# Kernel optimization log

Hardware: AMD Instinct MI355X
Metric: run time of the kernel (lower is better)

The kernel has to match this reference:

```python
import jax, jax.numpy as jnp
import numpy as np

B, S, D, H, SEP = 4, 2048, 768, 8, 102
Dh = D // H


def layer_norm(x, g, b, eps=1e-5):
    m = jnp.mean(x, axis=-1, keepdims=True)
    v = jnp.var(x, axis=-1, keepdims=True)
    return (x - m) / jnp.sqrt(v + eps) * g + b


def setup_inputs() -> dict:
    key = jax.random.key(0)
    ks = jax.random.split(key, 16)
    hidden_states = jax.random.normal(ks[0], (B, S, D), dtype=jnp.float32)
    # input_ids: random vocab ids avoiding SEP, with two SEP tokens planted per row
    rng = np.random.default_rng(0)
    ids = rng.integers(103, 30000, size=(B, S))
    for b in range(B):
        ids[b, S // 3 + 7 * b] = SEP
        ids[b, 2 * S // 3 + 11 * b] = SEP
    input_ids = jnp.asarray(ids, dtype=jnp.int64)
    attention_mask = jnp.ones((B, S), dtype=jnp.int32)
    sc = 0.02
    p = {}
    p['Wq'] = jax.random.normal(ks[1], (D, D), jnp.float32) * sc
    p['bq'] = jnp.zeros((D,), jnp.float32)
    p['Wk'] = jax.random.normal(ks[2], (D, D), jnp.float32) * sc
    p['bk'] = jnp.zeros((D,), jnp.float32)
    p['Wv'] = jax.random.normal(ks[3], (D, D), jnp.float32) * sc
    p['bv'] = jnp.zeros((D,), jnp.float32)
    p['Wo'] = jax.random.normal(ks[4], (D, D), jnp.float32) * sc
    p['bo'] = jnp.zeros((D,), jnp.float32)
    p['ln1_g'] = jnp.ones((D,), jnp.float32)
    p['ln1_b'] = jnp.zeros((D,), jnp.float32)
    p['W1'] = jax.random.normal(ks[5], (D, D), jnp.float32) * sc  # d_ff = d_model
    p['b1'] = jnp.zeros((D,), jnp.float32)
    p['W2'] = jax.random.normal(ks[6], (D, D), jnp.float32) * sc
    p['b2'] = jnp.zeros((D,), jnp.float32)
    p['ln2_g'] = jnp.ones((D,), jnp.float32)
    p['ln2_b'] = jnp.zeros((D,), jnp.float32)
    p['dn_g'] = jnp.ones((D,), jnp.float32)
    p['dn_b'] = jnp.zeros((D,), jnp.float32)
    return dict(hidden_states=hidden_states, input_ids=input_ids,
                attention_mask=attention_mask, **p)


def reference(hidden_states, input_ids, attention_mask,
              Wq, bq, Wk, bk, Wv, bv, Wo, bo, ln1_g, ln1_b,
              W1, b1, W2, b2, ln2_g, ln2_b, dn_g, dn_b):
    x = hidden_states
    # --- SEP-based ragged segment discovery (vectorized over batch) ---
    sep = input_ids == SEP                       # [B,S]
    idx = jnp.arange(S)
    big = S
    first = jnp.min(jnp.where(sep, idx, big), axis=-1)                       # [B]
    second = jnp.min(jnp.where(sep & (idx[None, :] > first[:, None]), idx, big), axis=-1)
    has2 = second < big                          # >= 2 SEP tokens present
    mid = S // 2
    src_end = jnp.where(has2, first, mid)
    hyp_start = jnp.where(has2, first + 1, mid)
    hyp_end = jnp.where(has2, second, S - 1)
    src_mask = (idx[None, :] >= 1) & (idx[None, :] < src_end[:, None])       # keys [B,S]
    hyp_mask = (idx[None, :] >= hyp_start[:, None]) & (idx[None, :] < hyp_end[:, None])
    valid = jnp.any(src_mask, -1) & jnp.any(hyp_mask, -1)                    # [B]

    # --- cross-attention: queries = hyp tokens, keys/values = src tokens ---
    q = (x @ Wq + bq).reshape(B, S, H, Dh)
    k = (x @ Wk + bk).reshape(B, S, H, Dh)
    v = (x @ Wv + bv).reshape(B, S, H, Dh)
    scores = jnp.einsum('bqhd,bkhd->bhqk', q, k) / jnp.sqrt(jnp.float32(Dh))
    scores = jnp.where(src_mask[:, None, None, :], scores, jnp.float32(-1e9))
    attn = jax.nn.softmax(scores, axis=-1)
    ctx = jnp.einsum('bhqk,bkhd->bqhd', attn, v).reshape(B, S, D)
    mha = ctx @ Wo + bo
    x1 = layer_norm(x + mha, ln1_g, ln1_b)
    ffn = jax.nn.gelu(x1 @ W1 + b1) @ W2 + b2
    x2 = layer_norm(x1 + ffn, ln2_g, ln2_b)      # updated_hyp

    # --- diff + LayerNorm, scatter back into hyp segment only ---
    diff = layer_norm(x2 - x, dn_g, dn_b)
    upd = hyp_mask & valid[:, None]
    return jnp.where(upd[..., None], x + diff, x)
```

## Files before the change

kernel.cpp:

```cpp
#include <hip/hip_runtime.h>
#include <math.h>

#define BB 4
#define SS 2048
#define DD 768
#define HH 8
#define DHD 96
#define SEP_ID 102
#define CHUNK 352
#define NCH_MAX 3
#define QT64 11
#define SLOTB 12800

typedef __attribute__((ext_vector_type(8))) short bf16x8;
typedef __attribute__((ext_vector_type(4))) float f32x4;

static __device__ __forceinline__ float gelu_tanh(float x) {
  float x3 = x * x * x;
  float t = tanhf(0.7978845608028654f * (x + 0.044715f * x3));
  return 0.5f * x * (1.0f + t);
}

static __device__ __forceinline__ unsigned short f2bf(float f) {
  unsigned int u = __float_as_uint(f);
  u = (u + 0x7FFF + ((u >> 16) & 1)) >> 16;
  return (unsigned short)u;
}

static __device__ __forceinline__ float bf2f(unsigned short u) {
  return __uint_as_float(((unsigned int)u) << 16);
}

#define MFMA16(A, B, C) __builtin_amdgcn_mfma_f32_16x16x32_bf16(A, B, C, 0, 0, 0)

static __device__ __forceinline__ void gl16(const void* g, void* l) {
  __builtin_amdgcn_global_load_lds(
      (__attribute__((address_space(1))) unsigned int*)g,
      (__attribute__((address_space(3))) unsigned int*)l, 16, 0, 0);
}

__global__ __launch_bounds__(256) void prep(
    const int* __restrict__ ids, int* __restrict__ seg,
    const float* __restrict__ x, unsigned short* __restrict__ xbf,
    float* __restrict__ out, int n4,
    const float* __restrict__ W0, const float* __restrict__ W1,
    const float* __restrict__ W2, const float* __restrict__ W3,
    const float* __restrict__ W4, const float* __restrict__ W5,
    unsigned short* __restrict__ Wt) {
  __shared__ char smem[64 * 65 * 4];
  int bx = blockIdx.x;
  if (bx < 4) {
    int* s1 = (int*)smem;
    int* s2 = s1 + 256;
    int b = bx;
    const int* row = ids + (size_t)b * SS;
    int m1 = SS, m2 = SS;
    for (int i = threadIdx.x; i < SS; i += 256) {
      if (row[i] == SEP_ID) {
        if (i < m1) { m2 = m1; m1 = i; }
        else if (i < m2) { m2 = i; }
      }
    }
    s1[threadIdx.x] = m1; s2[threadIdx.x] = m2;
    __syncthreads();
    for (int off = 128; off > 0; off >>= 1) {
      if (threadIdx.x < off) {
        int a1 = s1[threadIdx.x], a2 = s2[threadIdx.x];
        int b1 = s1[threadIdx.x + off], b2 = s2[threadIdx.x + off];
        s1[threadIdx.x] = min(a1, b1);
        s2[threadIdx.x] = min(max(a1, b1), min(a2, b2));
      }
      __syncthreads();
    }
    if (threadIdx.x == 0) {
      int first = s1[0], second = s2[0];
      bool has2 = (second < SS);
      int mid = SS / 2;
      int src_end = has2 ? first : mid;
      int hyp_lo = has2 ? (first + 1) : mid;
      int hyp_hi = has2 ? second : (SS - 1);
      int valid = ((src_end - 1) > 0 && (hyp_hi - hyp_lo) > 0) ? 1 : 0;
      if (!valid) { src_end = 1; hyp_lo = 0; hyp_hi = 0; }
      seg[b * 4 + 0] = src_end;
      seg[b * 4 + 1] = hyp_lo;
      seg[b * 4 + 2] = hyp_hi;
      seg[b * 4 + 3] = valid;
    }
  } else if (bx < 1540) {
    int i = (bx - 4) * 256 + threadIdx.x;
    int stride = 1536 * 256;
    const float4* xi = (const float4*)x;
    float4* oi = (float4*)out;
    for (; i < n4; i += stride) {
      float4 v = xi[i];
      oi[i] = v;
      ushort4 r;
      r.x = f2bf(v.x); r.y = f2bf(v.y); r.z = f2bf(v.z); r.w = f2bf(v.w);
      *(ushort4*)(xbf + (size_t)i * 4) = r;
    }
  } else {
    float (*t)[65] = (float(*)[65])smem;
    int idx = bx - 1540;
    int z = idx / 144, rem = idx - z * 144;
    const float* W = (z == 0) ? W0 : (z == 1) ? W1 : (z == 2) ? W2
                    : (z == 3) ? W3 : (z == 4) ? W4 : W5;
    unsigned short* O = Wt + (size_t)z * DD * DD;
    int k0 = (rem / 12) * 64, n0 = (rem % 12) * 64;
    for (int i = threadIdx.x; i < 4096; i += 256) {
      int kk = i >> 6, nn = i & 63;
      t[kk][nn] = W[(size_t)(k0 + kk) * DD + n0 + nn];
    }
    __syncthreads();
    for (int i = threadIdx.x; i < 4096; i += 256) {
      int nn = i >> 6, kk = i & 63;
      O[(size_t)(n0 + nn) * DD + k0 + kk] = f2bf(t[kk][nn]);
    }
  }
}

__device__ __forceinline__ void gemm_core(
    const unsigned short* __restrict__ A, const unsigned short* __restrict__ Wt,
    const float* __restrict__ bias, unsigned short* __restrict__ C,
    int b, int row0, int hi, int col0, int which, float rs,
    unsigned short (*Al)[64 * 64], unsigned short (*Bl)[64 * 64]) {
  int tid = threadIdx.x, w = tid >> 6, lane = tid & 63;
  int llo = lane & 15, lhi = lane >> 4;
  int wrg = w >> 1, wcg = w & 1;

  const unsigned short* Ab = A + (size_t)b * SS * DD;

  f32x4 acc[2][2];
#pragma unroll
  for (int i = 0; i < 2; ++i)
#pragma unroll
    for (int j = 0; j < 2; ++j) acc[i][j] = (f32x4){0.f, 0.f, 0.f, 0.f};

  auto STAGE = [&](int t, int buf) {
    int kk = t * 64;
#pragma unroll
    for (int j = 0; j < 2; ++j) {
      int s = j * 256 + tid;
      int row = s >> 3, c = s & 7;
      int gr = min(row0 + row, hi - 1);
      gl16(Ab + (size_t)gr * DD + kk + ((c ^ (row & 7)) * 8),
           &Al[buf][(size_t)(j * 256 + w * 64) * 8]);
    }
#pragma unroll
    for (int j = 0; j < 2; ++j) {
      int s = j * 256 + tid;
      int row = s >> 3, c = s & 7;
      gl16(Wt + (size_t)(col0 + row) * DD + kk + ((c ^ (row & 7)) * 8),
           &Bl[buf][(size_t)(j * 256 + w * 64) * 8]);
    }
  };

  STAGE(0, 0);
  __syncthreads();
  for (int t = 0; t < DD / 64; ++t) {
    int cur = t & 1;
    if (t + 1 < DD / 64) STAGE(t + 1, cur ^ 1);
#pragma unroll
    for (int ksub = 0; ksub < 2; ++ksub) {
      bf16x8 af[2], bfr[2];
#pragma unroll
      for (int mi = 0; mi < 2; ++mi) {
        int lr = wrg * 32 + mi * 16 + llo;
        int slot = lr * 8 + ((ksub * 4 + lhi) ^ (lr & 7));
        af[mi] = *(const bf16x8*)&Al[cur][(size_t)slot * 8];
      }
#pragma unroll
      for (int ni = 0; ni < 2; ++ni) {
        int lr = wcg * 32 + ni * 16 + llo;
        int slot = lr * 8 + ((ksub * 4 + lhi) ^ (lr & 7));
        bfr[ni] = *(const bf16x8*)&Bl[cur][(size_t)slot * 8];
      }
#pragma unroll
      for (int mi = 0; mi < 2; ++mi)
#pragma unroll
        for (int ni = 0; ni < 2; ++ni)
          acc[mi][ni] = MFMA16(af[mi], bfr[ni], acc[mi][ni]);
    }
    __syncthreads();
  }

#pragma unroll
  for (int mi = 0; mi < 2; ++mi)
#pragma unroll
    for (int ni = 0; ni < 2; ++ni) {
      int col = col0 + wcg * 32 + ni * 16 + llo;
      float bsv = bias[col];
      int rowb = row0 + wrg * 32 + mi * 16 + lhi * 4;
#pragma unroll
      for (int r = 0; r < 4; ++r) {
        int row = rowb + r;
        if (row < hi) {
          float v = (acc[mi][ni][r] + bsv) * rs;
          if (which == 4) v = gelu_tanh(v);
          C[((size_t)(b * SS + row)) * DD + col] = f2bf(v);
        }
      }
    }
}

__global__ __launch_bounds__(256) void gemm_qkv(
    const unsigned short* __restrict__ A, const unsigned short* __restrict__ Wt3,
    const float* __restrict__ bq, const float* __restrict__ bk, const float* __restrict__ bv,
    unsigned short* __restrict__ Qo, unsigned short* __restrict__ Ko,
    unsigned short* __restrict__ Vto, const int* __restrict__ seg, float rs) {
  __shared__ unsigned short Al[2][64 * 64];
  __shared__ unsigned short B0l[2][64 * 64];
  __shared__ unsigned short B1l[2][64 * 64];
  const size_t WSZ = (size_t)DD * DD;
  int b = blockIdx.z;
  int col0 = (blockIdx.x % 12) * 64;
  int tid = threadIdx.x, w = tid >> 6, lane = tid & 63;
  int llo = lane & 15, lhi = lane >> 4;
  int wrg = w >> 1, wcg = w & 1;
  const unsigned short* Ab = A + (size_t)b * SS * DD;

  if (blockIdx.x < 12) {
    int lo = seg[b * 4 + 1], hi = seg[b * 4 + 2];
    int row0 = lo + (int)blockIdx.y * 64;
    if (row0 >= hi) return;
    gemm_core(A, Wt3, bq, Qo, b, row0, hi, col0, 3, rs, Al, B0l);
    return;
  }

  int hi = seg[b * 4 + 0];
  int row0 = 1 + (int)blockIdx.y * 64;
  if (row0 >= hi + 64) return;
  const unsigned short* Wk_ = Wt3 + WSZ;
  const unsigned short* Wv_ = Wt3 + 2 * WSZ;

  f32x4 accK[2][2], accV[2][2];
#pragma unroll
  for (int i = 0; i < 2; ++i)
#pragma unroll
    for (int j = 0; j < 2; ++j) {
      accK[i][j] = (f32x4){0.f, 0.f, 0.f, 0.f};
      accV[i][j] = (f32x4){0.f, 0.f, 0.f, 0.f};
    }

  auto STAGE = [&](int t, int buf) {
    int kk = t * 64;
#pragma unroll
    for (int j = 0; j < 2; ++j) {
      int s = j * 256 + tid;
      int row = s >> 3, c = s & 7;
      int gr = min(row0 + row, hi - 1);
      gl16(Ab + (size_t)gr * DD + kk + ((c ^ (row & 7)) * 8),
           &Al[buf][(size_t)(j * 256 + w * 64) * 8]);
    }
#pragma unroll
    for (int j = 0; j < 2; ++j) {
      int s = j * 256 + tid;
      int row = s >> 3, c = s & 7;
      size_t woff = (size_t)(col0 + row) * DD + kk + ((c ^ (row & 7)) * 8);
      gl16(Wk_ + woff, &B0l[buf][(size_t)(j * 256 + w * 64) * 8]);
      gl16(Wv_ + woff, &B1l[buf][(size_t)(j * 256 + w * 64) * 8]);
    }
  };

  STAGE(0, 0);
  __syncthreads();
  for (int t = 0; t < DD / 64; ++t) {
    int cur = t & 1;
    if (t + 1 < DD / 64) STAGE(t + 1, cur ^ 1);
#pragma unroll
    for (int ksub = 0; ksub < 2; ++ksub) {
      bf16x8 af[2], bk2[2], bv2[2];
#pragma unroll
      for (int mi = 0; mi < 2; ++mi) {
        int lr = wrg * 32 + mi * 16 + llo;
        int slot = lr * 8 + ((ksub * 4 + lhi) ^ (lr & 7));
        af[mi] = *(const bf16x8*)&Al[cur][(size_t)slot * 8];
      }
#pragma unroll
      for (int ni = 0; ni < 2; ++ni) {
        int lr = wcg * 32 + ni * 16 + llo;
        int slot = lr * 8 + ((ksub * 4 + lhi) ^ (lr & 7));
        bk2[ni] = *(const bf16x8*)&B0l[cur][(size_t)slot * 8];
        bv2[ni] = *(const bf16x8*)&B1l[cur][(size_t)slot * 8];
      }
#pragma unroll
      for (int mi = 0; mi < 2; ++mi)
#pragma unroll
        for (int ni = 0; ni < 2; ++ni) {
          accK[mi][ni] = MFMA16(af[mi], bk2[ni], accK[mi][ni]);
          accV[mi][ni] = MFMA16(af[mi], bv2[ni], accV[mi][ni]);
        }
    }
    __syncthreads();
  }

#pragma unroll
  for (int mi = 0; mi < 2; ++mi)
#pragma unroll
    for (int ni = 0; ni < 2; ++ni) {
      int col = col0 + wcg * 32 + ni * 16 + llo;
      float bkv = bk[col], bvv = bv[col];
      int rowb = row0 + wrg * 32 + mi * 16 + lhi * 4;
#pragma unroll
      for (int r = 0; r < 4; ++r) {
        int row = rowb + r;
        if (row < hi)
          Ko[((size_t)(b * SS + row)) * DD + col] = f2bf(accK[mi][ni][r] + bkv);
        Vto[((size_t)b * DD + col) * SS + row] =
            (row < hi) ? f2bf(accV[mi][ni][r] + bvv) : (unsigned short)0;
      }
    }
}

__global__ __launch_bounds__(256) void gemm_mfma(
    const unsigned short* __restrict__ A, const unsigned short* __restrict__ Wt,
    const float* __restrict__ bias, unsigned short* __restrict__ C,
    const int* __restrict__ seg, int gelu) {
  __shared__ unsigned short Al[2][64 * 64];
  __shared__ unsigned short Bl[2][64 * 64];
  int b = blockIdx.z;
  int lo = seg[b * 4 + 1], hi = seg[b * 4 + 2];
  int row0 = lo + (int)blockIdx.y * 64;
  if (row0 >= hi) return;
  gemm_core(A, Wt, bias, C, b, row0, hi, (int)blockIdx.x * 64,
            gelu ? 4 : 3, 1.f, Al, Bl);
}

__global__ __launch_bounds__(256) void attn_split(
    const unsigned short* __restrict__ Q, const unsigned short* __restrict__ K,
    const unsigned short* __restrict__ Vt, char* __restrict__ part,
    const int* __restrict__ seg) {
  int bh = blockIdx.z;
  int b = bh >> 3, h = bh & 7;
  int src_hi = seg[b * 4 + 0];
  int hyp_lo = seg[b * 4 + 1], hyp_hi = seg[b * 4 + 2];
  int q0b = hyp_lo + (int)blockIdx.x * 64;
  if (q0b >= hyp_hi) return;
  int ks = 1 + (int)blockIdx.y * CHUNK;
  if (ks >= src_hi) return;
  int ke = min(ks + CHUNK, src_hi);

  __shared__ unsigned short kls[64 * 128];
  __shared__ unsigned short vls[96 * 64];
  __shared__ unsigned short plds[4][1024];

  int tid = threadIdx.x;
  int w = tid >> 6, lane = tid & 63;
  int llo = lane & 15, lhi = lane >> 4;

  int qrow = min(q0b + w * 16 + llo, hyp_hi - 1);
  const unsigned short* qbase = Q + ((size_t)(b * SS + qrow)) * DD + h * DHD;
  bf16x8 qf[3];
#pragma unroll
  for (int df = 0; df < 3; ++df)
    qf[df] = *(const bf16x8*)(qbase + df * 32 + lhi * 8);

  const unsigned short* Kb = K + (size_t)b * SS * DD + h * DHD;
  const unsigned short* Vb = Vt + ((size_t)b * DD + h * DHD) * SS;

  f32x4 acc[6];
#pragma unroll
  for (int dt = 0; dt < 6; ++dt) acc[dt] = (f32x4){0.f, 0.f, 0.f, 0.f};
  float m_r[4] = {-1e30f, -1e30f, -1e30f, -1e30f};
  float l_r[4] = {0.f, 0.f, 0.f, 0.f};

  for (int k0 = ks; k0 < ke; k0 += 64) {
    __syncthreads();
#pragma unroll
    for (int j = 0; j < 4; ++j) {
      int s = j * 256 + tid;
      int row = s >> 4, sl = s & 15;
      int c = sl ^ (row & 7);
      int krow = min(k0 + row, ke - 1);
      gl16(Kb + (size_t)krow * DD + c * 8,
           &kls[(size_t)(j * 256 + w * 64) * 8]);
    }
#pragma unroll
    for (int j = 0; j < 3; ++j) {
      int s = j * 256 + tid;
      int row = s >> 3, sl = s & 7;
      int c = sl ^ (row & 7);
      gl16(Vb + (size_t)row * SS + k0 + c * 8,
           &vls[(size_t)(j * 256 + w * 64) * 8]);
    }
    __syncthreads();
    f32x4 s[4];
    __builtin_amdgcn_s_setprio(1);
#pragma unroll
    for (int t = 0; t < 4; ++t) {
      f32x4 st = (f32x4){0.f, 0.f, 0.f, 0.f};
      int row = t * 16 + llo;
#pragma unroll
      for (int df = 0; df < 3; ++df) {
        int slot = df * 4 + lhi;
        bf16x8 kf = *(const bf16x8*)&kls[row * 128 + ((slot ^ (row & 7)) << 3)];
        st = MFMA16(qf[df], kf, st);
      }
      s[t] = st;
    }
    __builtin_amdgcn_s_setprio(0);
    float mx[4] = {-1e30f, -1e30f, -1e30f, -1e30f};
#pragma unroll
    for (int t = 0; t < 4; ++t) {
      bool kv = (k0 + t * 16 + llo) < ke;
#pragma unroll
      for (int r = 0; r < 4; ++r) {
        float sv = kv ? s[t][r] : -1e30f;
        s[t][r] = sv;
        mx[r] = fmaxf(mx[r], sv);
      }
    }
#pragma unroll
    for (int st = 1; st < 16; st <<= 1)
#pragma unroll
      for (int r = 0; r < 4; ++r) mx[r] = fmaxf(mx[r], __shfl_xor(mx[r], st));

    float p[4][4];
#pragma unroll
    for (int r = 0; r < 4; ++r) {
      float mn = fmaxf(m_r[r], mx[r]);
      float sc = __expf(m_r[r] - mn);
      m_r[r] = mn;
      l_r[r] *= sc;
#pragma unroll
      for (int dt = 0; dt < 6; ++dt) acc[dt][r] *= sc;
      float ps = 0.f;
#pragma unroll
      for (int t = 0; t < 4; ++t) {
        float pv = (s[t][r] > -1e29f) ? __expf(s[t][r] - mn) : 0.f;
        p[t][r] = pv;
        ps += pv;
      }
#pragma unroll
      for (int st = 1; st < 16; st <<= 1) ps += __shfl_xor(ps, st);
      l_r[r] += ps;
    }
#pragma unroll
    for (int t = 0; t < 4; ++t)
#pragma unroll
      for (int r = 0; r < 4; ++r) {
        int qq = lhi * 4 + r, kk = t * 16 + llo;
        plds[w][qq * 64 + (kk ^ ((qq & 7) << 3))] = f2bf(p[t][r]);
      }
    bf16x8 pa[2];
#pragma unroll
    for (int kh = 0; kh < 2; ++kh) {
      int idx = llo * 64 + ((lhi * 8 + kh * 32) ^ ((llo & 7) << 3));
      pa[kh] = *(const bf16x8*)&plds[w][idx];
    }
    __builtin_amdgcn_s_setprio(1);
#pragma unroll
    for (int dt = 0; dt < 6; ++dt) {
      int row = dt * 16 + llo;
#pragma unroll
      for (int kh = 0; kh < 2; ++kh) {
        int slot = kh * 4 + lhi;
        bf16x8 vf = *(const bf16x8*)&vls[row * 64 + ((slot ^ (row & 7)) << 3)];
        acc[dt] = MFMA16(pa[kh], vf, acc[dt]);
      }
    }
    __builtin_amdgcn_s_setprio(0);
  }
  char* slot = part + (((size_t)bh * QT64 + blockIdx.x) * NCH_MAX + blockIdx.y) * SLOTB;
  unsigned short* pacc = (unsigned short*)slot;
  float* pml = (float*)(slot + 12288);
#pragma unroll
  for (int r = 0; r < 4; ++r) {
    int qq = w * 16 + lhi * 4 + r;
#pragma unroll
    for (int dt = 0; dt < 6; ++dt)
      pacc[qq * 96 + dt * 16 + llo] = f2bf(acc[dt][r]);
    if (llo == 0) { pml[qq] = m_r[r]; pml[64 + qq] = l_r[r]; }
  }
}

__global__ __launch_bounds__(128) void attn_reduce(
    const char* __restrict__ part, unsigned short* __restrict__ ctx,
    const int* __restrict__ seg) {
  int bh = blockIdx.y;
  int b = bh >> 3, h = bh & 7;
  int src_hi = seg[b * 4 + 0];
  int hyp_lo = seg[b * 4 + 1], hyp_hi = seg[b * 4 + 2];
  int q0 = hyp_lo + (int)blockIdx.x * 16;
  if (q0 >= hyp_hi) return;
  int nch = (src_hi - 1 + CHUNK - 1) / CHUNK;
  if (nch > NCH_MAX) nch = NCH_MAX;
  int sub = blockIdx.x & 3;

  __shared__ float ml[NCH_MAX][32];
  __shared__ float Mg[16], invL[16], sc[NCH_MAX][16];
  int tid = threadIdx.x;
  const char* base = part + ((size_t)bh * QT64 + (blockIdx.x >> 2)) * NCH_MAX * SLOTB;
  for (int i = tid; i < 32 * nch; i += 128) {
    int c = i >> 5, j = i & 31;
    const float* pml = (const float*)(base + c * SLOTB + 12288);
    ml[c][j] = (j < 16) ? pml[sub * 16 + j] : pml[64 + sub * 16 + (j - 16)];
  }
  __syncthreads();
  if (tid < 16) {
    float mg = -1e30f;
    for (int c = 0; c < nch; ++c) mg = fmaxf(mg, ml[c][tid]);
    float lg = 0.f;
    for (int c = 0; c < nch; ++c) lg += ml[c][16 + tid] * __expf(ml[c][tid] - mg);
    Mg[tid] = mg;
    invL[tid] = 1.f / lg;
  }
  __syncthreads();
  for (int i = tid; i < 16 * nch; i += 128) {
    int c = i >> 4, q = i & 15;
    sc[c][q] = __expf(ml[c][q] - Mg[q]);
  }
  __syncthreads();
  for (int i = tid; i < 1536; i += 128) {
    int q = i / 96, d = i - q * 96;
    float v = 0.f;
    for (int c = 0; c < nch; ++c)
      v += bf2f(((const unsigned short*)(base + c * SLOTB))[(sub * 16 + q) * 96 + d]) * sc[c][q];
    int qq = q0 + q;
    if (qq < hyp_hi)
      ctx[((size_t)(b * SS + qq)) * DD + h * DHD + d] = f2bf(v * invL[q]);
  }
}

__device__ __forceinline__ float block_sum(float v, float* sbuf) {
#pragma unroll
  for (int off = 32; off > 0; off >>= 1) v += __shfl_xor(v, off);
  int lane = threadIdx.x & 63, w = threadIdx.x >> 6;
  __syncthreads();
  if (lane == 0) sbuf[w] = v;
  __syncthreads();
  return sbuf[0] + sbuf[1] + sbuf[2] + sbuf[3];
}

__global__ __launch_bounds__(256) void ln_residual(
    const float* __restrict__ X, const unsigned short* __restrict__ Yin,
    const float* __restrict__ g, const float* __restrict__ bta,
    float* __restrict__ Out, unsigned short* __restrict__ OutBf,
    const int* __restrict__ seg) {
  int b = blockIdx.y;
  int row = seg[b * 4 + 1] + (int)blockIdx.x;
  if (row >= seg[b * 4 + 2]) return;
  __shared__ float sbuf[4];
  size_t base = ((size_t)(b * SS + row)) * DD;
  int tid = threadIdx.x;
  float v[3];
  float sum = 0.f;
#pragma unroll
  for (int r = 0; r < 3; ++r) {
    int i = tid + r * 256;
    v[r] = X[base + i] + bf2f(Yin[base + i]);
    sum += v[r];
  }
  float mean = block_sum(sum, sbuf) * (1.f / DD);
  float vs = 0.f;
#pragma unroll
  for (int r = 0; r < 3; ++r) { float d = v[r] - mean; vs += d * d; }
  float var = block_sum(vs, sbuf) * (1.f / DD);
  float inv = rsqrtf(var + 1e-5f);
#pragma unroll
  for (int r = 0; r < 3; ++r) {
    int i = tid + r * 256;
    float o = (v[r] - mean) * inv * g[i] + bta[i];
    Out[base + i] = o;
    OutBf[base + i] = f2bf(o);
  }
}

__global__ __launch_bounds__(256) void ln2_diff_scatter(
    const float* __restrict__ X, const float* __restrict__ X1,
    const unsigned short* __restrict__ T2,
    const float* __restrict__ g2, const float* __restrict__ b2,
    const float* __restrict__ gd, const float* __restrict__ bd,
    float* __restrict__ Out, const int* __restrict__ seg) {
  int b = blockIdx.y;
  int row = seg[b * 4 + 1] + (int)blockIdx.x;
  if (row >= seg[b * 4 + 2]) return;
  size_t base = ((size_t)(b * SS + row)) * DD;
  int tid = threadIdx.x;
  __shared__ float sbuf[4];
  float y[3], xv[3];
  float sum = 0.f;
#pragma unroll
  for (int r = 0; r < 3; ++r) {
    int i = tid + r * 256;
    y[r] = X1[base + i] + bf2f(T2[base + i]);
    xv[r] = X[base + i];
    sum += y[r];
  }
  float mean = block_sum(sum, sbuf) * (1.f / DD);
  float vs = 0.f;
#pragma unroll
  for (int r = 0; r < 3; ++r) { float d = y[r] - mean; vs += d * d; }
  float var = block_sum(vs, sbuf) * (1.f / DD);
  float inv = rsqrtf(var + 1e-5f);
  float z[3];
  float sum2 = 0.f;
#pragma unroll
  for (int r = 0; r < 3; ++r) {
    int i = tid + r * 256;
    float x2 = (y[r] - mean) * inv * g2[i] + b2[i];
    z[r] = x2 - xv[r];
    sum2 += z[r];
  }
  float mean2 = block_sum(sum2, sbuf) * (1.f / DD);
  float vs2 = 0.f;
#pragma unroll
  for (int r = 0; r < 3; ++r) { float d = z[r] - mean2; vs2 += d * d; }
  float var2 = block_sum(vs2, sbuf) * (1.f / DD);
  float inv2 = rsqrtf(var2 + 1e-5f);
#pragma unroll
  for (int r = 0; r < 3; ++r) {
    int i = tid + r * 256;
    Out[base + i] = xv[r] + (z[r] - mean2) * inv2 * gd[i] + bd[i];
  }
}

extern "C" void kernel_launch(void* const* d_in, const int* in_sizes, int n_in,
                              void* d_out, int out_size, void* d_ws, size_t ws_size,
                              hipStream_t stream) {
  const float* x = (const float*)d_in[0];
  const int* ids = (const int*)d_in[1];
  const float* Wq = (const float*)d_in[3];
  const float* bq = (const float*)d_in[4];
  const float* Wk = (const float*)d_in[5];
  const float* bk = (const float*)d_in[6];
  const float* Wv = (const float*)d_in[7];
  const float* bv = (const float*)d_in[8];
  const float* Wo = (const float*)d_in[9];
  const float* bo = (const float*)d_in[10];
  const float* ln1g = (const float*)d_in[11];
  const float* ln1b = (const float*)d_in[12];
  const float* W1 = (const float*)d_in[13];
  const float* b1 = (const float*)d_in[14];
  const float* W2 = (const float*)d_in[15];
  const float* b2 = (const float*)d_in[16];
  const float* ln2g = (const float*)d_in[17];
  const float* ln2b = (const float*)d_in[18];
  const float* dng = (const float*)d_in[19];
  const float* dnb = (const float*)d_in[20];
  float* out = (float*)d_out;

  char* ws = (char*)d_ws;
  int* seg = (int*)ws;
  size_t NBH = (size_t)BB * SS * DD * 2;
  char* Ap = ws + 256;
  char* Bp = Ap + NBH;
  char* Cp = Bp + NBH;
  char* Dp = Cp + NBH;
  char* Fp = Dp + NBH + 8192;
  char* Gp = Fp + (size_t)BB * SS * DD * 4;

  unsigned short* x_bf = (unsigned short*)Ap;
  unsigned short* ctx_bf = (unsigned short*)Ap;
  unsigned short* h1_bf = (unsigned short*)Ap;
  unsigned short* q_bf = (unsigned short*)Bp;
  unsigned short* mha_bf = (unsigned short*)Bp;
  unsigned short* k_bf = (unsigned short*)Cp;
  unsigned short* t2_bf = (unsigned short*)Cp;
  unsigned short* vt_bf = (unsigned short*)Dp;
  unsigned short* x1_bf = (unsigned short*)Dp;
  char* part = Fp;
  float* x1f = (float*)Fp;
  unsigned short* wt = (unsigned short*)Gp;
  const size_t WSZ = (size_t)DD * DD;

  const float rs = 0.1020620726159658f;

  prep<<<2404, 256, 0, stream>>>(ids, seg, x, x_bf, out, BB * SS * DD / 4,
                                 Wq, Wk, Wv, Wo, W1, W2, wt);

  gemm_qkv<<<dim3(24, 12, BB), 256, 0, stream>>>(
      x_bf, wt, bq, bk, bv, q_bf, k_bf, vt_bf, seg, rs);

  attn_split<<<dim3(QT64, NCH_MAX, 32), 256, 0, stream>>>(q_bf, k_bf, vt_bf, part, seg);
  attn_reduce<<<dim3(44, 32), 128, 0, stream>>>(part, ctx_bf, seg);

  gemm_mfma<<<dim3(12, 11, BB), 256, 0, stream>>>(ctx_bf, wt + 3 * WSZ, bo, mha_bf, seg, 0);
  ln_residual<<<dim3(704, BB), 256, 0, stream>>>(x, mha_bf, ln1g, ln1b, x1f, x1_bf, seg);
  gemm_mfma<<<dim3(12, 11, BB), 256, 0, stream>>>(x1_bf, wt + 4 * WSZ, b1, h1_bf, seg, 1);
  gemm_mfma<<<dim3(12, 11, BB), 256, 0, stream>>>(h1_bf, wt + 5 * WSZ, b2, t2_bf, seg, 0);
  ln2_diff_scatter<<<dim3(704, BB), 256, 0, stream>>>(x, x1f, t2_bf, ln2g, ln2b, dng, dnb, out, seg);
}
```

Baseline: 150.5 us.

## Fuse split-attention reduction into Wo projection GEMM A-tile staging

Removes the separate attn_reduce kernel and the ctx intermediate buffer. The Wo GEMM now computes per-row softmax merge scales from the partial max and sum values. It combines the bf16 partial outputs on the fly while staging its A tiles into shared memory. This saves a launch and a global round trip, but the reduction work is repeated across the 12 column blocks and A-tile loads become synchronous, with register arithmetic in place of async copies.

```diff
diff --git a/kernel.cpp b/kernel.cpp
--- a/kernel.cpp
+++ b/kernel.cpp
@@ -325,6 +325,135 @@
             gelu ? 4 : 3, 1.f, Al, Bl);
 }
 
+__global__ __launch_bounds__(256) void gemm_wo(
+    const char* __restrict__ part, const unsigned short* __restrict__ Wt,
+    const float* __restrict__ bias, unsigned short* __restrict__ C,
+    const int* __restrict__ seg) {
+  __shared__ unsigned short Al[2][64 * 64];
+  __shared__ unsigned short Bl[2][64 * 64];
+  __shared__ float scl[8 * NCH_MAX * 64];
+  int b = blockIdx.z;
+  int src_hi = seg[b * 4 + 0];
+  int lo = seg[b * 4 + 1], hi = seg[b * 4 + 2];
+  int qt = blockIdx.y;
+  int row0 = lo + qt * 64;
+  if (row0 >= hi) return;
+  int col0 = (int)blockIdx.x * 64;
+  int nch = (src_hi - 1 + CHUNK - 1) / CHUNK;
+  if (nch > NCH_MAX) nch = NCH_MAX;
+
+  int tid = threadIdx.x, w = tid >> 6, lane = tid & 63;
+  int llo = lane & 15, lhi = lane >> 4;
+  int wrg = w >> 1, wcg = w & 1;
+
+  for (int hq = tid; hq < 512; hq += 256) {
+    int h = hq >> 6, q = hq & 63;
+    const char* pb = part + ((size_t)((b * 8 + h) * QT64 + qt) * NCH_MAX) * SLOTB;
+    float m0 = ((const float*)(pb + 12288))[q];
+    float l0 = ((const float*)(pb + 12288))[64 + q];
+    float m1 = -1e30f, l1 = 0.f, m2 = -1e30f, l2 = 0.f;
+    if (nch > 1) {
+      m1 = ((const float*)(pb + SLOTB + 12288))[q];
+      l1 = ((const float*)(pb + SLOTB + 12288))[64 + q];
+    }
+    if (nch > 2) {
+      m2 = ((const float*)(pb + 2 * SLOTB + 12288))[q];
+      l2 = ((const float*)(pb + 2 * SLOTB + 12288))[64 + q];
+    }
+    float mg = fmaxf(m0, fmaxf(m1, m2));
+    float s0 = __expf(m0 - mg);
+    float s1 = (nch > 1) ? __expf(m1 - mg) : 0.f;
+    float s2 = (nch > 2) ? __expf(m2 - mg) : 0.f;
+    float inv = 1.f / (l0 * s0 + l1 * s1 + l2 * s2);
+    scl[(h * NCH_MAX + 0) * 64 + q] = s0 * inv;
+    scl[(h * NCH_MAX + 1) * 64 + q] = s1 * inv;
+    scl[(h * NCH_MAX + 2) * 64 + q] = s2 * inv;
+  }
+  __syncthreads();
+
+  f32x4 acc[2][2];
+#pragma unroll
+  for (int i = 0; i < 2; ++i)
+#pragma unroll
+    for (int j = 0; j < 2; ++j) acc[i][j] = (f32x4){0.f, 0.f, 0.f, 0.f};
+
+  auto STAGE = [&](int t, int buf) {
+    int kk = t * 64;
+#pragma unroll
+    for (int jj = 0; jj < 2; ++jj) {
+      int s = jj * 256 + tid;
+      int row = s >> 3, cidx = s & 7;
+      int d = kk + cidx * 8;
+      int h = d / 96;
+      int dd = d - h * 96;
+      float va[8] = {0.f, 0.f, 0.f, 0.f, 0.f, 0.f, 0.f, 0.f};
+      const char* pb = part + ((size_t)((b * 8 + h) * QT64 + qt) * NCH_MAX) * SLOTB;
+      for (int c = 0; c < nch; ++c) {
+        const unsigned short* pp = (const unsigned short*)(pb + (size_t)c * SLOTB);
+        bf16x8 pv = *(const bf16x8*)(pp + row * 96 + dd);
+        float scv = scl[(h * NCH_MAX + c) * 64 + row];
+#pragma unroll
+        for (int j2 = 0; j2 < 8; ++j2) va[j2] += bf2f((unsigned short)pv[j2]) * scv;
+      }
+      unsigned short pk[8];
+#pragma unroll
+      for (int j2 = 0; j2 < 8; ++j2) pk[j2] = f2bf(va[j2]);
+      *(bf16x8*)&Al[buf][(size_t)(row * 8 + (cidx ^ (row & 7))) * 8] = *(bf16x8*)pk;
+    }
+#pragma unroll
+    for (int jj = 0; jj < 2; ++jj) {
+      int s = jj * 256 + tid;
+      int row = s >> 3, c = s & 7;
+      gl16(Wt + (size_t)(col0 + row) * DD + kk + ((c ^ (row & 7)) * 8),
+           &Bl[buf][(size_t)(jj * 256 + w * 64) * 8]);
+    }
+  };
+
+  STAGE(0, 0);
+  __syncthreads();
+  for (int t = 0; t < DD / 64; ++t) {
+    int cur = t & 1;
+    if (t + 1 < DD / 64) STAGE(t + 1, cur ^ 1);
+#pragma unroll
+    for (int ksub = 0; ksub < 2; ++ksub) {
+      bf16x8 af[2], bfr[2];
+#pragma unroll
+      for (int mi = 0; mi < 2; ++mi) {
+        int lr = wrg * 32 + mi * 16 + llo;
+        int slot = lr * 8 + ((ksub * 4 + lhi) ^ (lr & 7));
+        af[mi] = *(const bf16x8*)&Al[cur][(size_t)slot * 8];
+      }
+#pragma unroll
+      for (int ni = 0; ni < 2; ++ni) {
+        int lr = wcg * 32 + ni * 16 + llo;
+        int slot = lr * 8 + ((ksub * 4 + lhi) ^ (lr & 7));
+        bfr[ni] = *(const bf16x8*)&Bl[cur][(size_t)slot * 8];
+      }
+#pragma unroll
+      for (int mi = 0; mi < 2; ++mi)
+#pragma unroll
+        for (int ni = 0; ni < 2; ++ni)
+          acc[mi][ni] = MFMA16(af[mi], bfr[ni], acc[mi][ni]);
+    }
+    __syncthreads();
+  }
+
+#pragma unroll
+  for (int mi = 0; mi < 2; ++mi)
+#pragma unroll
+    for (int ni = 0; ni < 2; ++ni) {
+      int col = col0 + wcg * 32 + ni * 16 + llo;
+      float bsv = bias[col];
+      int rowb = row0 + wrg * 32 + mi * 16 + lhi * 4;
+#pragma unroll
+      for (int r = 0; r < 4; ++r) {
+        int row = rowb + r;
+        if (row < hi)
+          C[((size_t)(b * SS + row)) * DD + col] = f2bf(acc[mi][ni][r] + bsv);
+      }
+    }
+}
+
 __global__ __launch_bounds__(256) void attn_split(
     const unsigned short* __restrict__ Q, const unsigned short* __restrict__ K,
     const unsigned short* __restrict__ Vt, char* __restrict__ part,
@@ -470,54 +599,6 @@
     for (int dt = 0; dt < 6; ++dt)
       pacc[qq * 96 + dt * 16 + llo] = f2bf(acc[dt][r]);
     if (llo == 0) { pml[qq] = m_r[r]; pml[64 + qq] = l_r[r]; }
-  }
-}
-
-__global__ __launch_bounds__(128) void attn_reduce(
-    const char* __restrict__ part, unsigned short* __restrict__ ctx,
-    const int* __restrict__ seg) {
-  int bh = blockIdx.y;
-  int b = bh >> 3, h = bh & 7;
-  int src_hi = seg[b * 4 + 0];
-  int hyp_lo = seg[b * 4 + 1], hyp_hi = seg[b * 4 + 2];
-  int q0 = hyp_lo + (int)blockIdx.x * 16;
-  if (q0 >= hyp_hi) return;
-  int nch = (src_hi - 1 + CHUNK - 1) / CHUNK;
-  if (nch > NCH_MAX) nch = NCH_MAX;
-  int sub = blockIdx.x & 3;
-
-  __shared__ float ml[NCH_MAX][32];
-  __shared__ float Mg[16], invL[16], sc[NCH_MAX][16];
-  int tid = threadIdx.x;
-  const char* base = part + ((size_t)bh * QT64 + (blockIdx.x >> 2)) * NCH_MAX * SLOTB;
-  for (int i = tid; i < 32 * nch; i += 128) {
-    int c = i >> 5, j = i & 31;
-    const float* pml = (const float*)(base + c * SLOTB + 12288);
-    ml[c][j] = (j < 16) ? pml[sub * 16 + j] : pml[64 + sub * 16 + (j - 16)];
-  }
-  __syncthreads();
-  if (tid < 16) {
-    float mg = -1e30f;
-    for (int c = 0; c < nch; ++c) mg = fmaxf(mg, ml[c][tid]);
-    float lg = 0.f;
-    for (int c = 0; c < nch; ++c) lg += ml[c][16 + tid] * __expf(ml[c][tid] - mg);
-    Mg[tid] = mg;
-    invL[tid] = 1.f / lg;
-  }
-  __syncthreads();
-  for (int i = tid; i < 16 * nch; i += 128) {
-    int c = i >> 4, q = i & 15;
-    sc[c][q] = __expf(ml[c][q] - Mg[q]);
-  }
-  __syncthreads();
-  for (int i = tid; i < 1536; i += 128) {
-    int q = i / 96, d = i - q * 96;
-    float v = 0.f;
-    for (int c = 0; c < nch; ++c)
-      v += bf2f(((const unsigned short*)(base + c * SLOTB))[(sub * 16 + q) * 96 + d]) * sc[c][q];
-    int qq = q0 + q;
-    if (qq < hyp_hi)
-      ctx[((size_t)(b * SS + qq)) * DD + h * DHD + d] = f2bf(v * invL[q]);
   }
 }
 
@@ -650,7 +731,6 @@
   char* Gp = Fp + (size_t)BB * SS * DD * 4;
 
   unsigned short* x_bf = (unsigned short*)Ap;
-  unsigned short* ctx_bf = (unsigned short*)Ap;
   unsigned short* h1_bf = (unsigned short*)Ap;
   unsigned short* q_bf = (unsigned short*)Bp;
   unsigned short* mha_bf = (unsigned short*)Bp;
@@ -672,9 +752,9 @@
       x_bf, wt, bq, bk, bv, q_bf, k_bf, vt_bf, seg, rs);
 
   attn_split<<<dim3(QT64, NCH_MAX, 32), 256, 0, stream>>>(q_bf, k_bf, vt_bf, part, seg);
-  attn_reduce<<<dim3(44, 32), 128, 0, stream>>>(part, ctx_bf, seg);
-
-  gemm_mfma<<<dim3(12, 11, BB), 256, 0, stream>>>(ctx_bf, wt + 3 * WSZ, bo, mha_bf, seg, 0);
+
+  gemm_wo<<<dim3(12, 11, BB), 256, 0, stream>>>(part, wt + 3 * WSZ, bo, mha_bf, seg);
+
   ln_residual<<<dim3(704, BB), 256, 0, stream>>>(x, mha_bf, ln1g, ln1b, x1f, x1_bf, seg);
   gemm_mfma<<<dim3(12, 11, BB), 256, 0, stream>>>(x1_bf, wt + 4 * WSZ, b1, h1_bf, seg, 1);
   gemm_mfma<<<dim3(12, 11, BB), 256, 0, stream>>>(h1_bf, wt + 5 * WSZ, b2, t2_bf, seg, 0);
```

New measurement: 154.9 us. 1.03x slower.
